# Kernel optimization log

Hardware: AMD Instinct MI355X
Metric: run time of the kernel (lower is better)

The kernel has to match this reference:

```python
import jax, jax.numpy as jnp
import numpy as np

B, N, C, H, P = 8, 4096, 512, 8, 64
D = C // H


def setup_inputs() -> dict:
    key = jax.random.key(0)
    ks = jax.random.split(key, 5)
    s = 0.02
    return {
        "x": jax.random.normal(ks[0], (B, N, C), jnp.float32),
        "w_qkv": jax.random.normal(ks[1], (3 * C, C), jnp.float32) * s,
        "w_e": jax.random.normal(ks[2], (P, N), jnp.float32) * s,
        "b_e": jnp.zeros((P,), jnp.float32),
        "temperature": jnp.ones((1, 1, 1), jnp.float32),
        "temperature2": jnp.ones((H, 1, 1), jnp.float32),
        "w_o1": jax.random.normal(ks[3], (C // 2, C), jnp.float32) * s,
        "b_o1": jnp.zeros((C // 2,), jnp.float32),
        "w_o2": jax.random.normal(ks[4], (C // 2, C), jnp.float32) * s,
        "b_o2": jnp.zeros((C // 2,), jnp.float32),
    }


def reference(x, w_qkv, w_e, b_e, temperature, temperature2, w_o1, b_o1, w_o2, b_o2):
    Bs, Ns, Cs = x.shape
    # qkvv projection and head split: [B,N,3C] -> [3,B,H,N,D]
    qkv = (x @ w_qkv.T).reshape(Bs, Ns, 3, H, D)
    qkv = jnp.transpose(qkv, (2, 0, 3, 1, 4))
    q, k, v = qkv[0], qkv[1], qkv[2]
    q_t = jnp.swapaxes(q, -2, -1)  # [B,H,D,N]
    k_t = jnp.swapaxes(k, -2, -1)  # [B,H,D,N]
    v_t = jnp.swapaxes(v, -2, -1)  # [B,H,D,N]
    # Linformer-style projection along token axis; E = F (shared weights)
    kp = k_t @ w_e.T + b_e  # [B,H,D,P]
    vp = v_t @ w_e.T + b_e  # [B,H,D,P]
    # L2-normalize q along tokens (k is normalized in the original AFTER
    # projection, so that normalization is dead code and omitted)
    qn = q_t / jnp.maximum(jnp.linalg.norm(q_t, axis=-1, keepdims=True), 1e-12)
    # ---- channel attention: [B,C,C] scores over raw x ----
    xt = jnp.swapaxes(x, -2, -1)  # [B,C,N]
    attn_ca = jax.nn.softmax((xt @ x) * temperature, axis=-1)
    x_ca = jnp.swapaxes(attn_ca @ xt, -2, -1)  # [B,N,C]
    # ---- projected spatial attention: [B,H,N,P] scores ----
    attn_sa = jax.nn.softmax(
        jnp.einsum('bhdn,bhdp->bhnp', qn, kp) * temperature2, axis=-1)
    x_sa = jnp.einsum('bhnp,bhdp->bhnd', attn_sa, vp)  # [B,H,N,D]
    # faithful to torch: permute(0,3,1,2) then reshape(B,N,C)
    x_sa = jnp.transpose(x_sa, (0, 3, 1, 2)).reshape(Bs, Ns, Cs)
    out = jnp.concatenate(
        [x_sa @ w_o1.T + b_o1, x_ca @ w_o2.T + b_o2], axis=-1)
    return out
```

## Files before the change

kernel.cpp:

```cpp
#include <hip/hip_runtime.h>
#include <hip/hip_bf16.h>

typedef unsigned short u16;

#define AS1 __attribute__((address_space(1)))
#define AS3 __attribute__((address_space(3)))

static __device__ __forceinline__ float bl(u16 v) {
    return __uint_as_float(((unsigned)v) << 16);
}
static __device__ __forceinline__ u16 f2b(float f) {
    unsigned u = __float_as_uint(f);
    unsigned r = u + 0x7FFFu + ((u >> 16) & 1u);
    return (u16)(r >> 16);
}
static __device__ __forceinline__ float ldf(const void* p, long i, int isbf) {
    if (isbf) return bl(((const u16*)p)[i]);
    return ((const float*)p)[i];
}
static __device__ __forceinline__ void gload_lds16(const u16* g, u16* l) {
    __builtin_amdgcn_global_load_lds((const AS1 void*)g, (AS3 void*)l, 16, 0, 0);
}

typedef __attribute__((ext_vector_type(8))) short bf16x8;
typedef __attribute__((ext_vector_type(4))) float f32x4;

static __device__ __forceinline__ bf16x8 pack8(const float* p) {
    const float4 x0 = ((const float4*)p)[0];
    const float4 x1 = ((const float4*)p)[1];
    unsigned r0, r1, r2, r3;
    asm("v_cvt_pk_bf16_f32 %0, %1, %2" : "=v"(r0) : "v"(x0.x), "v"(x0.y));
    asm("v_cvt_pk_bf16_f32 %0, %1, %2" : "=v"(r1) : "v"(x0.z), "v"(x0.w));
    asm("v_cvt_pk_bf16_f32 %0, %1, %2" : "=v"(r2) : "v"(x1.x), "v"(x1.y));
    asm("v_cvt_pk_bf16_f32 %0, %1, %2" : "=v"(r3) : "v"(x1.z), "v"(x1.w));
    union { unsigned u[4]; bf16x8 v; } u;
    u.u[0] = r0; u.u[1] = r1; u.u[2] = r2; u.u[3] = r3;
    return u.v;
}

__global__ void dtype_probe(const void* __restrict__ temp, unsigned* __restrict__ flag) {
    if (threadIdx.x == 0 && blockIdx.x == 0)
        flag[0] = (((const u16*)temp)[0] == 0x3F80) ? 1u : 0u;
}

__global__ __launch_bounds__(256) void zero_f32(float* __restrict__ p, long n) {
    const long stride = (long)gridDim.x * 256;
    for (long i = (long)blockIdx.x * 256 + threadIdx.x; i < n; i += stride)
        p[i] = 0.f;
}

__global__ __launch_bounds__(256) void conv_x(const void* __restrict__ X,
                                              u16* __restrict__ xb,
                                              u16* __restrict__ xt,
                                              const unsigned* __restrict__ flg)
{
    __shared__ u16 tile[64][65];
    const int f = (int)flg[0];
    const int b = blockIdx.z;
    const int n0 = blockIdx.x * 64, c0 = blockIdx.y * 64;
    const int t = threadIdx.x, r0 = t >> 6, c = t & 63;
    #pragma unroll
    for (int rr = 0; rr < 16; ++rr) {
        const int r = rr * 4 + r0;
        const long gi = ((long)b * 4096 + n0 + r) * 512 + c0 + c;
        const u16 h = f2b(ldf(X, gi, f));
        xb[gi] = h;
        tile[r][c] = h;
    }
    __syncthreads();
    #pragma unroll
    for (int rr = 0; rr < 16; ++rr) {
        const int cc = rr * 4 + r0;
        xt[((long)b * 512 + c0 + cc) * 4096 + n0 + c] = tile[c][cc];
    }
}

__global__ __launch_bounds__(256) void conv_w(const void* __restrict__ W,
                                              u16* __restrict__ wb, long nelem,
                                              const unsigned* __restrict__ flg)
{
    const int f = (int)flg[0];
    const long stride = (long)gridDim.x * 256;
    for (long i = (long)blockIdx.x * 256 + threadIdx.x; i < nelem; i += stride)
        wb[i] = f2b(ldf(W, i, f));
}

__global__ __launch_bounds__(256) void gemm_mfma_nt(
    const u16* __restrict__ A, const u16* __restrict__ B,
    void* __restrict__ C, const void* __restrict__ bias,
    int M, int N, int K, int lda, int ldb, int ldc,
    long sA, long sB, long sC,
    const unsigned* __restrict__ flg, int biasExt, int cF32, int kSplit,
    float* __restrict__ qsq)
{
    __shared__ u16 Asm[2][128 * 32];
    __shared__ u16 Bsm[2][128 * 32];
    const int t = threadIdx.x, w = t >> 6, l = t & 63;
    const int gx = gridDim.x, gy = gridDim.y;
    const long nwg = (long)gx * gy * gridDim.z;
    const long lin = blockIdx.x + (long)gx * (blockIdx.y + (long)gy * blockIdx.z);
    long nid = lin;
    if ((nwg & 7) == 0) nid = (lin & 7) * (nwg >> 3) + (lin >> 3);
    const int by = (int)(nid % gy);
    const long r2 = nid / gy;
    const int bx = (int)(r2 % gx);
    int bz = (int)(r2 / gx), kz = 0;
    if (kSplit > 1) { kz = bz % kSplit; bz /= kSplit; }
    const u16* Ab = A + (long)bz * sA;
    const u16* Bb = B + (long)bz * sB;
    const int m0 = bx * 128, n0 = by * 128;
    const int wm = (w >> 1) * 64, wn = (w & 1) * 64;
    const int srow = l >> 2;
    const int scol = (l & 3) * 8;
    const int fr = l & 15;
    const int fk = (l >> 4) * 8;
    f32x4 acc[4][4];
    #pragma unroll
    for (int i = 0; i < 4; ++i)
        #pragma unroll
        for (int j = 0; j < 4; ++j)
            acc[i][j] = (f32x4){0.f, 0.f, 0.f, 0.f};

    const int kChunk = K / kSplit;
    const int kBeg = kz * kChunk, kEnd = kBeg + kChunk;
    const int q0 = w, q1 = w + 4;

#define STAGE(nb, kk)                                                                   \
    do {                                                                                \
        gload_lds16(Ab + (long)(m0 + q0 * 16 + srow) * lda + (kk) + scol, &Asm[nb][q0 * 512]); \
        gload_lds16(Ab + (long)(m0 + q1 * 16 + srow) * lda + (kk) + scol, &Asm[nb][q1 * 512]); \
        gload_lds16(Bb + (long)(n0 + q0 * 16 + srow) * ldb + (kk) + scol, &Bsm[nb][q0 * 512]); \
        gload_lds16(Bb + (long)(n0 + q1 * 16 + srow) * ldb + (kk) + scol, &Bsm[nb][q1 * 512]); \
    } while (0)

    STAGE(0, kBeg);
    __syncthreads();
    int cur = 0;
    for (int k0 = kBeg; k0 < kEnd; k0 += 32) {
        if (k0 + 32 < kEnd) STAGE(cur ^ 1, k0 + 32);
        bf16x8 af[4], bf[4];
        #pragma unroll
        for (int i = 0; i < 4; ++i) {
            af[i] = *(const bf16x8*)&Asm[cur][(wm + i * 16 + fr) * 32 + fk];
            bf[i] = *(const bf16x8*)&Bsm[cur][(wn + i * 16 + fr) * 32 + fk];
        }
        #pragma unroll
        for (int i = 0; i < 4; ++i)
            #pragma unroll
            for (int j = 0; j < 4; ++j)
                acc[i][j] = __builtin_amdgcn_mfma_f32_16x16x32_bf16(af[i], bf[j], acc[i][j], 0, 0, 0);
        __syncthreads();
        cur ^= 1;
    }
#undef STAGE

    const int f = (int)flg[0];
    const long cOff = (long)bz * sC;
    float bj[4] = {0.f, 0.f, 0.f, 0.f};
    if (bias) {
        #pragma unroll
        for (int j = 0; j < 4; ++j)
            bj[j] = ldf(bias, n0 + wn + j * 16 + fr, biasExt ? f : 1);
    }
    #pragma unroll
    for (int i = 0; i < 4; ++i) {
        #pragma unroll
        for (int j = 0; j < 4; ++j) {
            const int col = n0 + wn + j * 16 + fr;
            #pragma unroll
            for (int r = 0; r < 4; ++r) {
                const int row = m0 + wm + i * 16 + (l >> 4) * 4 + r;
                const float v = acc[i][j][r] + bj[j];
                if (kSplit > 1)
                    atomicAdd(&((float*)C)[cOff + (long)row * ldc + col], v);
                else if (cF32)
                    ((float*)C)[cOff + (long)row * ldc + col] = v;
                else
                    ((u16*)C)[cOff + (long)row * ldc + col] = f2b(v);
            }
        }
    }
    if (qsq) {
        #pragma unroll
        for (int j = 0; j < 4; ++j) {
            const int col = n0 + wn + j * 16 + fr;
            if (col < 512) {
                float s = 0.f;
                #pragma unroll
                for (int i = 0; i < 4; ++i)
                    #pragma unroll
                    for (int r = 0; r < 4; ++r)
                        s = fmaf(acc[i][j][r], acc[i][j][r], s);
                s += __shfl_xor(s, 16, 64);
                s += __shfl_xor(s, 32, 64);
                if ((l >> 4) == 0)
                    atomicAdd(&qsq[(long)bz * 512 + col], s);
            }
        }
    }
}

__global__ __launch_bounds__(512, 2) void gemm256_nt(
    const u16* __restrict__ A, const u16* __restrict__ B,
    void* __restrict__ C, const void* __restrict__ bias,
    int K, int lda, int ldb, int ldc,
    long sA, long sB, long sC,
    const unsigned* __restrict__ flg, int biasExt, int cF32,
    float* __restrict__ qsq,
    const u16* __restrict__ A2, const u16* __restrict__ B2,
    const void* __restrict__ bias2, int nSwitch)
{
    __shared__ u16 Asm[2][256 * 32];
    __shared__ u16 Bsm[2][256 * 32];
    const int t = threadIdx.x, w = t >> 6, l = t & 63;
    const int gx = gridDim.x, gy = gridDim.y;
    const long nwg = (long)gx * gy * gridDim.z;
    const long lin = blockIdx.x + (long)gx * (blockIdx.y + (long)gy * blockIdx.z);
    long nid = lin;
    if ((nwg & 7) == 0) nid = (lin & 7) * (nwg >> 3) + (lin >> 3);
    const int by = (int)(nid % gy);
    const long r2 = nid / gy;
    const int bx = (int)(r2 % gx);
    const int bz = (int)(r2 / gx);
    const int m0 = bx * 256, n0 = by * 256;
    const u16* Asel = A; const u16* Bsel = B; const void* bsel = bias;
    int nLoc = n0;
    if (A2 && n0 >= nSwitch) { Asel = A2; Bsel = B2; bsel = bias2; nLoc = n0 - nSwitch; }
    const u16* Ab = Asel + (long)bz * sA;
    const u16* Bb = Bsel + (long)bz * sB + (long)nLoc * ldb;
    const int wm = (w >> 1) * 64, wn = (w & 1) * 128;
    const int srow = l >> 2;
    const int selem = (((l & 3) ^ (srow & 3)) << 3);
    const int fr = l & 15;
    const int fk = (l >> 4) * 8;
    const int xorv = (fr & 3) << 3;
    f32x4 acc[4][8];
    #pragma unroll
    for (int i = 0; i < 4; ++i)
        #pragma unroll
        for (int j = 0; j < 8; ++j)
            acc[i][j] = (f32x4){0.f, 0.f, 0.f, 0.f};

#define STAGE256(nb, kk)                                                                     \
    do {                                                                                     \
        gload_lds16(Ab + (long)(m0 + w * 16 + srow) * lda + (kk) + selem, &Asm[nb][w * 512]);        \
        gload_lds16(Ab + (long)(m0 + (w + 8) * 16 + srow) * lda + (kk) + selem, &Asm[nb][(w + 8) * 512]); \
        gload_lds16(Bb + (long)(w * 16 + srow) * ldb + (kk) + selem, &Bsm[nb][w * 512]);             \
        gload_lds16(Bb + (long)((w + 8) * 16 + srow) * ldb + (kk) + selem, &Bsm[nb][(w + 8) * 512]);     \
    } while (0)

    STAGE256(0, 0);
    __syncthreads();
    int cur = 0;
    for (int k0 = 0; k0 < K; k0 += 32) {
        if (k0 + 32 < K) STAGE256(cur ^ 1, k0 + 32);
        bf16x8 af[4], bf[8];
        #pragma unroll
        for (int i = 0; i < 4; ++i)
            af[i] = *(const bf16x8*)&Asm[cur][((wm + i * 16 + fr) << 5) + (fk ^ xorv)];
        #pragma unroll
        for (int j = 0; j < 8; ++j)
            bf[j] = *(const bf16x8*)&Bsm[cur][((wn + j * 16 + fr) << 5) + (fk ^ xorv)];
        #pragma unroll
        for (int i = 0; i < 4; ++i)
            #pragma unroll
            for (int j = 0; j < 8; ++j)
                acc[i][j] = __builtin_amdgcn_mfma_f32_16x16x32_bf16(af[i], bf[j], acc[i][j], 0, 0, 0);
        __syncthreads();
        cur ^= 1;
    }
#undef STAGE256

    const int f = (int)flg[0];
    const long cOff = (long)bz * sC;
    float bj[8];
    #pragma unroll
    for (int j = 0; j < 8; ++j) bj[j] = 0.f;
    if (bsel) {
        #pragma unroll
        for (int j = 0; j < 8; ++j)
            bj[j] = ldf(bsel, (nLoc & 255) + wn + j * 16 + fr, biasExt ? f : 1);
    }
    #pragma unroll
    for (int i = 0; i < 4; ++i) {
        #pragma unroll
        for (int j = 0; j < 8; ++j) {
            const int col = n0 + wn + j * 16 + fr;
            #pragma unroll
            for (int r = 0; r < 4; ++r) {
                const int row = m0 + wm + i * 16 + (l >> 4) * 4 + r;
                const float v = acc[i][j][r] + bj[j];
                if (cF32) ((float*)C)[cOff + (long)row * ldc + col] = v;
                else      ((u16*)C)[cOff + (long)row * ldc + col] = f2b(v);
            }
        }
    }
    if (qsq) {
        #pragma unroll
        for (int j = 0; j < 8; ++j) {
            const int col = n0 + wn + j * 16 + fr;
            if (col < 512) {
                float s = 0.f;
                #pragma unroll
                for (int i = 0; i < 4; ++i)
                    #pragma unroll
                    for (int r = 0; r < 4; ++r)
                        s = fmaf(acc[i][j][r], acc[i][j][r], s);
                s += __shfl_xor(s, 16, 64);
                s += __shfl_xor(s, 32, 64);
                if ((l >> 4) == 0)
                    atomicAdd(&qsq[(long)bz * 512 + col], s);
            }
        }
    }
}

__global__ __launch_bounds__(256) void xe_mfma(const u16* __restrict__ WEB,
                                               const u16* __restrict__ XT,
                                               float* __restrict__ XE)
{
    const int t = threadIdx.x, w = t >> 6, l = t & 63;
    const int l15 = l & 15, g = l >> 4;
    const int c0 = blockIdx.x * 128 + (w >> 1) * 64;
    const int b = blockIdx.y;
    const int nbase = blockIdx.z * 512 + (w & 1) * 256;
    f32x4 acc[4][4];
    #pragma unroll
    for (int i = 0; i < 4; ++i)
        #pragma unroll
        for (int j = 0; j < 4; ++j)
            acc[i][j] = (f32x4){0.f, 0.f, 0.f, 0.f};
    for (int ks = 0; ks < 8; ++ks) {
        const int n = nbase + ks * 32 + g * 8;
        bf16x8 a[4], bb[4];
        #pragma unroll
        for (int i = 0; i < 4; ++i)
            a[i] = *(const bf16x8*)&WEB[(long)(i * 16 + l15) * 4096 + n];
        #pragma unroll
        for (int j = 0; j < 4; ++j)
            bb[j] = *(const bf16x8*)&XT[((long)b * 512 + c0 + j * 16 + l15) * 4096 + n];
        #pragma unroll
        for (int i = 0; i < 4; ++i)
            #pragma unroll
            for (int j = 0; j < 4; ++j)
                acc[i][j] = __builtin_amdgcn_mfma_f32_16x16x32_bf16(a[i], bb[j], acc[i][j], 0, 0, 0);
    }
    #pragma unroll
    for (int i = 0; i < 4; ++i)
        #pragma unroll
        for (int j = 0; j < 4; ++j)
            #pragma unroll
            for (int r = 0; r < 4; ++r)
                atomicAdd(&XE[((long)b * 64 + i * 16 + g * 4 + r) * 512 + c0 + j * 16 + l15],
                          acc[i][j][r]);
}

__global__ __launch_bounds__(256) void kpvp2_mfma(const float* __restrict__ XE,
                                                  const u16* __restrict__ WQB,
                                                  const float* __restrict__ qsq,
                                                  const void* __restrict__ be,
                                                  const void* __restrict__ temp2,
                                                  u16* __restrict__ kpT,
                                                  u16* __restrict__ vpB,
                                                  const unsigned* __restrict__ flg)
{
    __shared__ float lds[4][4096];
    const int bh = blockIdx.x, b = bh >> 3, h = bh & 7;
    const int t = threadIdx.x, w = t >> 6, l = t & 63;
    const int l15 = l & 15, g = l >> 4;
    const int isV = w >> 1;
    const int ch = w & 1;
    const u16* wrow = WQB + (long)(512 + isV * 512 + h * 64) * 512;
    const float* xr = XE + (long)b * 64 * 512;
    f32x4 acc[4][4];
    #pragma unroll
    for (int i = 0; i < 4; ++i)
        #pragma unroll
        for (int j = 0; j < 4; ++j)
            acc[i][j] = (f32x4){0.f, 0.f, 0.f, 0.f};
    for (int ks = 0; ks < 8; ++ks) {
        const int c = ch * 256 + ks * 32 + g * 8;
        bf16x8 a[4], bb[4];
        if (!isV) {
            #pragma unroll
            for (int i = 0; i < 4; ++i)
                a[i] = pack8(&xr[(long)(i * 16 + l15) * 512 + c]);
            #pragma unroll
            for (int j = 0; j < 4; ++j)
                bb[j] = *(const bf16x8*)&wrow[(long)(j * 16 + l15) * 512 + c];
        } else {
            #pragma unroll
            for (int i = 0; i < 4; ++i)
                a[i] = *(const bf16x8*)&wrow[(long)(i * 16 + l15) * 512 + c];
            #pragma unroll
            for (int j = 0; j < 4; ++j)
                bb[j] = pack8(&xr[(long)(j * 16 + l15) * 512 + c]);
        }
        #pragma unroll
        for (int i = 0; i < 4; ++i)
            #pragma unroll
            for (int j = 0; j < 4; ++j)
                acc[i][j] = __builtin_amdgcn_mfma_f32_16x16x32_bf16(a[i], bb[j], acc[i][j], 0, 0, 0);
    }
    #pragma unroll
    for (int i = 0; i < 4; ++i)
        #pragma unroll
        for (int j = 0; j < 4; ++j)
            #pragma unroll
            for (int r = 0; r < 4; ++r)
                lds[w][(i * 16 + g * 4 + r) * 64 + j * 16 + l15] = acc[i][j][r];
    __syncthreads();
    const int f = (int)flg[0];
    if (t < 128) {
        const float t2 = ldf(temp2, h, f);
        for (int e = t; e < 4096; e += 128) {
            const int p = e >> 6, d = e & 63;
            const float rn = 1.0f / fmaxf(sqrtf(qsq[b * 512 + h * 64 + d]), 1e-12f);
            kpT[(long)bh * 4096 + e] = f2b((lds[0][e] + lds[1][e] + ldf(be, p, f)) * rn * t2);
        }
    } else {
        for (int e = t - 128; e < 4096; e += 128) {
            vpB[(long)bh * 4096 + e] = f2b(lds[2][e] + lds[3][e] + ldf(be, e & 63, f));
        }
    }
}

__global__ __launch_bounds__(256) void softmax_ca(const float* __restrict__ S,
                                                  u16* __restrict__ A,
                                                  const void* __restrict__ temp,
                                                  const unsigned* __restrict__ flg)
{
    __shared__ float red[256];
    const int row = blockIdx.x;
    const int t = threadIdx.x;
    const float tv = ldf(temp, 0, (int)flg[0]);
    const float* s = S + (long)row * 512;
    float v0 = s[t] * tv;
    float v1 = s[t + 256] * tv;
    red[t] = fmaxf(v0, v1);
    __syncthreads();
    for (int o = 128; o > 0; o >>= 1) {
        if (t < o) red[t] = fmaxf(red[t], red[t + o]);
        __syncthreads();
    }
    const float m = red[0];
    __syncthreads();
    float e0 = expf(v0 - m), e1 = expf(v1 - m);
    red[t] = e0 + e1;
    __syncthreads();
    for (int o = 128; o > 0; o >>= 1) {
        if (t < o) red[t] += red[t + o];
        __syncthreads();
    }
    const float inv = 1.0f / red[0];
    u16* a = A + (long)row * 512;
    a[t]       = f2b(e0 * inv);
    a[t + 256] = f2b(e1 * inv);
}

__global__ __launch_bounds__(256) void spatial_attn_mfma(
    const u16* __restrict__ Q, const u16* __restrict__ kpT,
    const u16* __restrict__ vpB, u16* __restrict__ XSA)
{
    __shared__ u16 P[4][4096];
    const int bh = blockIdx.y, b = bh >> 3, h = bh & 7;
    const int t = threadIdx.x, w = t >> 6, l = t & 63;
    const int l15 = l & 15, g = l >> 4;
    const int n0 = blockIdx.x * 256 + w * 64;
    char* Pw = (char*)&P[w][0];

    const u16* kb = kpT + (long)bh * 4096;
    const u16* vb = vpB + (long)bh * 4096;
    bf16x8 akp[2][4], avp[2][4];
    #pragma unroll
    for (int ks = 0; ks < 2; ++ks)
        #pragma unroll
        for (int i = 0; i < 4; ++i) {
            akp[ks][i] = *(const bf16x8*)&kb[(i * 16 + l15) * 64 + ks * 32 + g * 8];
            avp[ks][i] = *(const bf16x8*)&vb[(i * 16 + l15) * 64 + ks * 32 + g * 8];
        }

    f32x4 sacc[4][4];
    #pragma unroll
    for (int i = 0; i < 4; ++i)
        #pragma unroll
        for (int j = 0; j < 4; ++j)
            sacc[i][j] = (f32x4){0.f, 0.f, 0.f, 0.f};
    const u16* qb = Q + ((long)b * 4096 + n0) * 512 + h * 64;
    #pragma unroll
    for (int ks = 0; ks < 2; ++ks) {
        bf16x8 bq[4];
        #pragma unroll
        for (int j = 0; j < 4; ++j)
            bq[j] = *(const bf16x8*)&qb[(long)(j * 16 + l15) * 512 + ks * 32 + g * 8];
        #pragma unroll
        for (int i = 0; i < 4; ++i)
            #pragma unroll
            for (int j = 0; j < 4; ++j)
                sacc[i][j] = __builtin_amdgcn_mfma_f32_16x16x32_bf16(akp[ks][i], bq[j], sacc[i][j], 0, 0, 0);
    }

    #pragma unroll
    for (int j = 0; j < 4; ++j) {
        float m = sacc[0][j][0];
        #pragma unroll
        for (int i = 0; i < 4; ++i)
            #pragma unroll
            for (int r = 0; r < 4; ++r)
                m = fmaxf(m, sacc[i][j][r]);
        m = fmaxf(m, __shfl_xor(m, 16, 64));
        m = fmaxf(m, __shfl_xor(m, 32, 64));
        float s = 0.f;
        #pragma unroll
        for (int i = 0; i < 4; ++i)
            #pragma unroll
            for (int r = 0; r < 4; ++r) {
                const float e = __expf(sacc[i][j][r] - m);
                sacc[i][j][r] = e;
                s += e;
            }
        s += __shfl_xor(s, 16, 64);
        s += __shfl_xor(s, 32, 64);
        const float inv = 1.0f / s;
        const int n = j * 16 + l15;
        const int swz = (n & 7) << 4;
        #pragma unroll
        for (int i = 0; i < 4; ++i) {
            unsigned lo, hi;
            float p0 = sacc[i][j][0] * inv, p1 = sacc[i][j][1] * inv;
            float p2 = sacc[i][j][2] * inv, p3 = sacc[i][j][3] * inv;
            asm("v_cvt_pk_bf16_f32 %0, %1, %2" : "=v"(lo) : "v"(p0), "v"(p1));
            asm("v_cvt_pk_bf16_f32 %0, %1, %2" : "=v"(hi) : "v"(p2), "v"(p3));
            const int byte = (n * 128 + i * 32 + g * 8) ^ swz;
            *(uint2*)(Pw + byte) = make_uint2(lo, hi);
        }
    }

    f32x4 oacc[4][4];
    #pragma unroll
    for (int i = 0; i < 4; ++i)
        #pragma unroll
        for (int j = 0; j < 4; ++j)
            oacc[i][j] = (f32x4){0.f, 0.f, 0.f, 0.f};
    #pragma unroll
    for (int ks = 0; ks < 2; ++ks) {
        bf16x8 bp[4];
        #pragma unroll
        for (int j = 0; j < 4; ++j) {
            const int n = j * 16 + l15;
            const int byte = (n * 128 + ks * 64 + g * 16) ^ ((n & 7) << 4);
            bp[j] = *(const bf16x8*)(Pw + byte);
        }
        #pragma unroll
        for (int i = 0; i < 4; ++i)
            #pragma unroll
            for (int j = 0; j < 4; ++j)
                oacc[i][j] = __builtin_amdgcn_mfma_f32_16x16x32_bf16(avp[ks][i], bp[j], oacc[i][j], 0, 0, 0);
    }

    const int rowoff = h * 8 + (n0 >> 9);
    const int colbase = n0 & 511;
    #pragma unroll
    for (int i = 0; i < 4; ++i)
        #pragma unroll
        for (int r = 0; r < 4; ++r) {
            const int d = i * 16 + g * 4 + r;
            u16* orow = XSA + ((long)b * 4096 + d * 64 + rowoff) * 512 + colbase;
            #pragma unroll
            for (int j = 0; j < 4; ++j)
                orow[j * 16 + l15] = f2b(oacc[i][j][r]);
        }
}

extern "C" void kernel_launch(void* const* d_in, const int* in_sizes, int n_in,
                              void* d_out, int out_size, void* d_ws, size_t ws_size,
                              hipStream_t stream)
{
    const void* x     = d_in[0];
    const void* w_qkv = d_in[1];
    const void* w_e   = d_in[2];
    const void* b_e   = d_in[3];
    const void* temp  = d_in[4];
    const void* temp2 = d_in[5];
    const void* w_o1  = d_in[6];
    const void* b_o1  = d_in[7];
    const void* w_o2  = d_in[8];
    const void* b_o2  = d_in[9];
    float* out = (float*)d_out;

    char* ws = (char*)d_ws;
    unsigned* flag = (unsigned*)ws; ws += 256;
    u16*   qb     = (u16*)ws;   ws += (size_t)8 * 4096 * 512 * 2;
    float* qsq    = (float*)ws; ws += (size_t)4096 * 4;
    float* xe     = (float*)ws; ws += (size_t)8 * 64 * 512 * 4;
    float* scores = (float*)ws; ws += (size_t)8 * 512 * 512 * 4;
    u16*   attn   = (u16*)ws;   ws += (size_t)8 * 512 * 512 * 2;
    u16*   x_ca   = (u16*)ws;   ws += (size_t)8 * 4096 * 512 * 2;
    u16*   xt     = (u16*)ws;   ws += (size_t)8 * 512 * 4096 * 2;
    u16*   xb     = (u16*)ws;   ws += (size_t)8 * 4096 * 512 * 2;
    u16*   wqb    = (u16*)ws;   ws += (size_t)1536 * 512 * 2;
    u16*   web    = (u16*)ws;   ws += (size_t)64 * 4096 * 2;
    u16*   wo1b   = (u16*)ws;   ws += (size_t)256 * 512 * 2;
    u16*   wo2b   = (u16*)ws;   ws += (size_t)256 * 512 * 2;
    u16*   kpT    = (u16*)ws;   ws += (size_t)262144 * 2;
    u16*   vpB    = (u16*)ws;   ws += (size_t)262144 * 2;
    u16*   x_sa   = xt;

    dtype_probe<<<1, 64, 0, stream>>>(temp, flag);
    conv_x<<<dim3(64, 8, 8), 256, 0, stream>>>(x, xb, xt, flag);
    conv_w<<<768, 256, 0, stream>>>(w_qkv, wqb, 1536L * 512, flag);
    conv_w<<<128, 256, 0, stream>>>(w_e, web, 64L * 4096, flag);
    conv_w<<<128, 256, 0, stream>>>(w_o1, wo1b, 256L * 512, flag);
    conv_w<<<128, 256, 0, stream>>>(w_o2, wo2b, 256L * 512, flag);
    zero_f32<<<4, 256, 0, stream>>>(qsq, 4096);
    gemm256_nt<<<dim3(16, 2, 8), 512, 0, stream>>>(
        xb, wqb, qb, nullptr, 512, 512, 512, 512,
        (long)4096 * 512, 0, (long)4096 * 512, flag, 0, 0, qsq,
        nullptr, nullptr, nullptr, 1 << 30);
    zero_f32<<<128, 256, 0, stream>>>(xe, (long)8 * 64 * 512);
    xe_mfma<<<dim3(4, 8, 8), 256, 0, stream>>>(web, xt, xe);
    kpvp2_mfma<<<64, 256, 0, stream>>>(xe, wqb, qsq, b_e, temp2, kpT, vpB, flag);
    zero_f32<<<2048, 256, 0, stream>>>(scores, (long)8 * 512 * 512);
    gemm_mfma_nt<<<dim3(4, 4, 32), 256, 0, stream>>>(
        xt, xt, scores, nullptr, 512, 512, 4096, 4096, 4096, 512,
        (long)512 * 4096, (long)512 * 4096, (long)512 * 512, flag, 0, 1, 4, nullptr);
    softmax_ca<<<4096, 256, 0, stream>>>(scores, attn, temp, flag);
    gemm256_nt<<<dim3(16, 2, 8), 512, 0, stream>>>(
        xb, attn, x_ca, nullptr, 512, 512, 512, 512,
        (long)4096 * 512, (long)512 * 512, (long)4096 * 512, flag, 0, 0, nullptr,
        nullptr, nullptr, nullptr, 1 << 30);
    spatial_attn_mfma<<<dim3(16, 64), 256, 0, stream>>>(qb, kpT, vpB, x_sa);
    gemm256_nt<<<dim3(16, 2, 8), 512, 0, stream>>>(
        x_sa, wo1b, out, b_o1, 512, 512, 512, 512,
        (long)4096 * 512, 0, (long)4096 * 512, flag, 1, 1, nullptr,
        x_ca, wo2b, b_o2, 256);
}
```

Measured before the change: 378.4 us.

## Exploit Gram matrix symmetry with 256-tile kernel for channel-attention scores

Replaces the generic split-K 128x128 GEMM computing x^T x with a dedicated 256x256-tile kernel that computes only the two diagonal blocks and one off-diagonal block per batch, mirroring the off-diagonal result into the transposed position. Diagonal tiles load one operand and reuse it for both sides, and the LDS layout uses an XOR swizzle to reduce bank conflicts. This removes about a quarter of the MFMA work and global loads for the score matrix. In exchange the grid shrinks to 96 blocks, which may underfill the GPU, and off-diagonal tiles issue twice the atomic adds.

```diff
diff --git a/kernel.cpp b/kernel.cpp
--- a/kernel.cpp
+++ b/kernel.cpp
@@ -83,121 +83,6 @@
     const long stride = (long)gridDim.x * 256;
     for (long i = (long)blockIdx.x * 256 + threadIdx.x; i < nelem; i += stride)
         wb[i] = f2b(ldf(W, i, f));
-}
-
-__global__ __launch_bounds__(256) void gemm_mfma_nt(
-    const u16* __restrict__ A, const u16* __restrict__ B,
-    void* __restrict__ C, const void* __restrict__ bias,
-    int M, int N, int K, int lda, int ldb, int ldc,
-    long sA, long sB, long sC,
-    const unsigned* __restrict__ flg, int biasExt, int cF32, int kSplit,
-    float* __restrict__ qsq)
-{
-    __shared__ u16 Asm[2][128 * 32];
-    __shared__ u16 Bsm[2][128 * 32];
-    const int t = threadIdx.x, w = t >> 6, l = t & 63;
-    const int gx = gridDim.x, gy = gridDim.y;
-    const long nwg = (long)gx * gy * gridDim.z;
-    const long lin = blockIdx.x + (long)gx * (blockIdx.y + (long)gy * blockIdx.z);
-    long nid = lin;
-    if ((nwg & 7) == 0) nid = (lin & 7) * (nwg >> 3) + (lin >> 3);
-    const int by = (int)(nid % gy);
-    const long r2 = nid / gy;
-    const int bx = (int)(r2 % gx);
-    int bz = (int)(r2 / gx), kz = 0;
-    if (kSplit > 1) { kz = bz % kSplit; bz /= kSplit; }
-    const u16* Ab = A + (long)bz * sA;
-    const u16* Bb = B + (long)bz * sB;
-    const int m0 = bx * 128, n0 = by * 128;
-    const int wm = (w >> 1) * 64, wn = (w & 1) * 64;
-    const int srow = l >> 2;
-    const int scol = (l & 3) * 8;
-    const int fr = l & 15;
-    const int fk = (l >> 4) * 8;
-    f32x4 acc[4][4];
-    #pragma unroll
-    for (int i = 0; i < 4; ++i)
-        #pragma unroll
-        for (int j = 0; j < 4; ++j)
-            acc[i][j] = (f32x4){0.f, 0.f, 0.f, 0.f};
-
-    const int kChunk = K / kSplit;
-    const int kBeg = kz * kChunk, kEnd = kBeg + kChunk;
-    const int q0 = w, q1 = w + 4;
-
-#define STAGE(nb, kk)                                                                   \
-    do {                                                                                \
-        gload_lds16(Ab + (long)(m0 + q0 * 16 + srow) * lda + (kk) + scol, &Asm[nb][q0 * 512]); \
-        gload_lds16(Ab + (long)(m0 + q1 * 16 + srow) * lda + (kk) + scol, &Asm[nb][q1 * 512]); \
-        gload_lds16(Bb + (long)(n0 + q0 * 16 + srow) * ldb + (kk) + scol, &Bsm[nb][q0 * 512]); \
-        gload_lds16(Bb + (long)(n0 + q1 * 16 + srow) * ldb + (kk) + scol, &Bsm[nb][q1 * 512]); \
-    } while (0)
-
-    STAGE(0, kBeg);
-    __syncthreads();
-    int cur = 0;
-    for (int k0 = kBeg; k0 < kEnd; k0 += 32) {
-        if (k0 + 32 < kEnd) STAGE(cur ^ 1, k0 + 32);
-        bf16x8 af[4], bf[4];
-        #pragma unroll
-        for (int i = 0; i < 4; ++i) {
-            af[i] = *(const bf16x8*)&Asm[cur][(wm + i * 16 + fr) * 32 + fk];
-            bf[i] = *(const bf16x8*)&Bsm[cur][(wn + i * 16 + fr) * 32 + fk];
-        }
-        #pragma unroll
-        for (int i = 0; i < 4; ++i)
-            #pragma unroll
-            for (int j = 0; j < 4; ++j)
-                acc[i][j] = __builtin_amdgcn_mfma_f32_16x16x32_bf16(af[i], bf[j], acc[i][j], 0, 0, 0);
-        __syncthreads();
-        cur ^= 1;
-    }
-#undef STAGE
-
-    const int f = (int)flg[0];
-    const long cOff = (long)bz * sC;
-    float bj[4] = {0.f, 0.f, 0.f, 0.f};
-    if (bias) {
-        #pragma unroll
-        for (int j = 0; j < 4; ++j)
-            bj[j] = ldf(bias, n0 + wn + j * 16 + fr, biasExt ? f : 1);
-    }
-    #pragma unroll
-    for (int i = 0; i < 4; ++i) {
-        #pragma unroll
-        for (int j = 0; j < 4; ++j) {
-            const int col = n0 + wn + j * 16 + fr;
-            #pragma unroll
-            for (int r = 0; r < 4; ++r) {
-                const int row = m0 + wm + i * 16 + (l >> 4) * 4 + r;
-                const float v = acc[i][j][r] + bj[j];
-                if (kSplit > 1)
-                    atomicAdd(&((float*)C)[cOff + (long)row * ldc + col], v);
-                else if (cF32)
-                    ((float*)C)[cOff + (long)row * ldc + col] = v;
-                else
-                    ((u16*)C)[cOff + (long)row * ldc + col] = f2b(v);
-            }
-        }
-    }
-    if (qsq) {
-        #pragma unroll
-        for (int j = 0; j < 4; ++j) {
-            const int col = n0 + wn + j * 16 + fr;
-            if (col < 512) {
-                float s = 0.f;
-                #pragma unroll
-                for (int i = 0; i < 4; ++i)
-                    #pragma unroll
-                    for (int r = 0; r < 4; ++r)
-                        s = fmaf(acc[i][j][r], acc[i][j][r], s);
-                s += __shfl_xor(s, 16, 64);
-                s += __shfl_xor(s, 32, 64);
-                if ((l >> 4) == 0)
-                    atomicAdd(&qsq[(long)bz * 512 + col], s);
-            }
-        }
-    }
 }
 
 __global__ __launch_bounds__(512, 2) void gemm256_nt(
@@ -315,6 +200,82 @@
     }
 }
 
+__global__ __launch_bounds__(512, 2) void gram256_sym(
+    const u16* __restrict__ XT, float* __restrict__ S)
+{
+    __shared__ u16 Asm[2][256 * 32];
+    __shared__ u16 Bsm[2][256 * 32];
+    const int t = threadIdx.x, w = t >> 6, l = t & 63;
+    const int tx = blockIdx.x, b = blockIdx.y, kz = blockIdx.z;
+    const int diag = (tx != 1);
+    const int m0 = (tx == 2) ? 256 : 0;
+    const int n0 = (tx == 0) ? 0 : 256;
+    const u16* Ab = XT + (long)b * 512 * 4096 + (long)m0 * 4096;
+    const u16* Bb = XT + (long)b * 512 * 4096 + (long)n0 * 4096;
+    const int wm = (w >> 1) * 64, wn = (w & 1) * 128;
+    const int srow = l >> 2;
+    const int selem = (((l & 3) ^ (srow & 3)) << 3);
+    const int fr = l & 15;
+    const int fk = (l >> 4) * 8;
+    const int xorv = (fr & 3) << 3;
+    f32x4 acc[4][8];
+    #pragma unroll
+    for (int i = 0; i < 4; ++i)
+        #pragma unroll
+        for (int j = 0; j < 8; ++j)
+            acc[i][j] = (f32x4){0.f, 0.f, 0.f, 0.f};
+
+#define GSTAGE(nb, kk)                                                                       \
+    do {                                                                                     \
+        gload_lds16(Ab + (long)(w * 16 + srow) * 4096 + (kk) + selem, &Asm[nb][w * 512]);            \
+        gload_lds16(Ab + (long)((w + 8) * 16 + srow) * 4096 + (kk) + selem, &Asm[nb][(w + 8) * 512]);    \
+        if (!diag) {                                                                         \
+            gload_lds16(Bb + (long)(w * 16 + srow) * 4096 + (kk) + selem, &Bsm[nb][w * 512]);        \
+            gload_lds16(Bb + (long)((w + 8) * 16 + srow) * 4096 + (kk) + selem, &Bsm[nb][(w + 8) * 512]); \
+        }                                                                                    \
+    } while (0)
+
+    const int kBeg = kz * 1024, kEnd = kBeg + 1024;
+    GSTAGE(0, kBeg);
+    __syncthreads();
+    int cur = 0;
+    for (int k0 = kBeg; k0 < kEnd; k0 += 32) {
+        if (k0 + 32 < kEnd) GSTAGE(cur ^ 1, k0 + 32);
+        const u16* Bsrc = diag ? &Asm[cur][0] : &Bsm[cur][0];
+        bf16x8 af[4], bf[8];
+        #pragma unroll
+        for (int i = 0; i < 4; ++i)
+            af[i] = *(const bf16x8*)&Asm[cur][((wm + i * 16 + fr) << 5) + (fk ^ xorv)];
+        #pragma unroll
+        for (int j = 0; j < 8; ++j)
+            bf[j] = *(const bf16x8*)&Bsrc[((wn + j * 16 + fr) << 5) + (fk ^ xorv)];
+        #pragma unroll
+        for (int i = 0; i < 4; ++i)
+            #pragma unroll
+            for (int j = 0; j < 8; ++j)
+                acc[i][j] = __builtin_amdgcn_mfma_f32_16x16x32_bf16(af[i], bf[j], acc[i][j], 0, 0, 0);
+        __syncthreads();
+        cur ^= 1;
+    }
+#undef GSTAGE
+
+    float* Sb = S + (long)b * 262144;
+    #pragma unroll
+    for (int i = 0; i < 4; ++i) {
+        #pragma unroll
+        for (int j = 0; j < 8; ++j) {
+            const int col = n0 + wn + j * 16 + fr;
+            #pragma unroll
+            for (int r = 0; r < 4; ++r) {
+                const int row = m0 + wm + i * 16 + (l >> 4) * 4 + r;
+                const float v = acc[i][j][r];
+                atomicAdd(&Sb[(long)row * 512 + col], v);
+                if (!diag) atomicAdd(&Sb[(long)col * 512 + row], v);
+            }
+        }
+    }
+}
+
 __global__ __launch_bounds__(256) void xe_mfma(const u16* __restrict__ WEB,
                                                const u16* __restrict__ XT,
                                                float* __restrict__ XE)
@@ -621,9 +582,7 @@
     xe_mfma<<<dim3(4, 8, 8), 256, 0, stream>>>(web, xt, xe);
     kpvp2_mfma<<<64, 256, 0, stream>>>(xe, wqb, qsq, b_e, temp2, kpT, vpB, flag);
     zero_f32<<<2048, 256, 0, stream>>>(scores, (long)8 * 512 * 512);
-    gemm_mfma_nt<<<dim3(4, 4, 32), 256, 0, stream>>>(
-        xt, xt, scores, nullptr, 512, 512, 4096, 4096, 4096, 512,
-        (long)512 * 4096, (long)512 * 4096, (long)512 * 512, flag, 0, 1, 4, nullptr);
+    gram256_sym<<<dim3(3, 8, 4), 512, 0, stream>>>(xt, scores);
     softmax_ca<<<4096, 256, 0, stream>>>(scores, attn, temp, flag);
     gemm256_nt<<<dim3(16, 2, 8), 512, 0, stream>>>(
         xb, attn, x_ca, nullptr, 512, 512, 512, 512,
```

Measured after the change: 417.3 us. 10.3% more time.
